# Kernel tuning notes

Hardware: AMD Instinct MI355X
Metric: run time of the kernel (lower is better)

## Reference

```python
import jax, jax.numpy as jnp
import numpy as np

B, S = 128, 32
C = [4, 8, 16, 32]
DN = ('NDHWC', 'DHWIO', 'NDHWC')


def _conv(x, w, stride=1, pad=None):
    k = w.shape[0]
    if pad is None:
        pad = [((k - 1) // 2, k // 2)] * 3  # k=3 -> (1,1); k=4 -> (1,2) as in scn even-kernel convention
    return jax.lax.conv_general_dilated(x, w, (stride,) * 3, pad, dimension_numbers=DN)


def _bn_relu(x, g, b, mask, eps=1e-4):
    # BatchNormLeakyReLU with leakiness=0 (ReLU); stats over ACTIVE voxels only, per channel
    cnt = jnp.maximum(mask.sum(), 1.0)
    mean = (x * mask).sum(axis=(0, 1, 2, 3)) / cnt
    var = (((x - mean) ** 2) * mask).sum(axis=(0, 1, 2, 3)) / cnt
    y = (x - mean) * jax.lax.rsqrt(var + eps) * g + b
    return jnp.maximum(y, 0.0) * mask


def _pool_mask(m):
    # scn.Convolution k=2 s=2: output site active iff any input in its 2^3 receptive field is active
    return jax.lax.reduce_window(m, 0.0, jax.lax.max, (1, 2, 2, 2, 1), (1, 2, 2, 2, 1), 'VALID')


def _up_mask(m):
    # scn.FullConvolution k=2 s=2: each active input activates its full 2^3 output block
    return jnp.repeat(jnp.repeat(jnp.repeat(m, 2, 1), 2, 2), 2, 3)


def _encoder(vox, maskraw, wp, enc, dec, wo):
    mask = (maskraw == 0).astype(vox.dtype)
    x = vox * mask
    x = _conv(x, wp) * mask  # prepare: submanifold conv 1 -> m=4
    for (g, b, ws, wd) in enc:  # 3 non-empty encoding stages (i < num_strides-1)
        x = _bn_relu(x, g, b, mask)
        x = _conv(x, ws) * mask               # submanifold conv k=3
        x = _conv(x, wd, stride=2, pad=[(0, 0)] * 3)  # strided Convolution k=2 s=2
        mask = _pool_mask(mask)
        x = x * mask
    # SparseToDense + view(-1, C*s^3) in NCDHW layout
    hidden = jnp.transpose(x, (0, 4, 1, 2, 3)).reshape(x.shape[0], -1)
    for (g, b, wu, ws3, ws4) in dec:  # i = 2, 1, 0
        x = _bn_relu(x, g, b, mask)
        x = jax.lax.conv_transpose(x, wu, (2, 2, 2), 'VALID', dimension_numbers=DN)  # FullConvolution
        mask = _up_mask(mask)
        x = x * mask
        x = _conv(x, ws3) * mask              # submanifold conv k=3 (end of decoding_conv1)
        mask = mask * (x[..., :1] > 0).astype(x.dtype)  # SparsifyFCS (applied twice; idempotent)
        x = x * mask
        x = _conv(x, ws4) * mask              # submanifold conv k=4 (decoding_conv2)
    out = _conv(x, wo) * mask                 # output: submanifold conv m -> 1
    return hidden, out


def setup_inputs():
    key = jax.random.key(0)
    ks = iter(jax.random.split(key, 64))

    def rnd(shape, s=0.1):
        return jax.random.normal(next(ks), shape, jnp.float32) * s

    inp = {}
    inp['vox'] = jax.random.normal(next(ks), (B, S, S, S, 1), jnp.float32)
    inp['maskraw'] = jax.random.randint(next(ks), (B, S, S, S, 1), 0, 10, jnp.int32)
    inp['wp'] = rnd((3, 3, 3, 1, C[0]))
    for i in range(3):
        ci, co = C[i], C[i + 1]
        inp[f'g_e{i}'] = 1.0 + rnd((ci,))
        inp[f'b_e{i}'] = rnd((ci,))
        inp[f'ws_e{i}'] = rnd((3, 3, 3, ci, ci))
        inp[f'wd_e{i}'] = rnd((2, 2, 2, ci, co))
    for j, i in enumerate([2, 1, 0]):
        ci, co = C[i + 1], C[i]
        inp[f'g_d{j}'] = 1.0 + rnd((ci,))
        inp[f'b_d{j}'] = rnd((ci,))
        inp[f'wu_d{j}'] = rnd((2, 2, 2, ci, co))
        inp[f'ws3_d{j}'] = rnd((3, 3, 3, co, co))
        inp[f'ws4_d{j}'] = rnd((4, 4, 4, co, co))
    inp['wo'] = rnd((3, 3, 3, C[0], 1))
    return inp


def reference(vox, maskraw, wp, g_e0, b_e0, ws_e0, wd_e0, g_e1, b_e1, ws_e1, wd_e1, g_e2, b_e2, ws_e2, wd_e2, g_d0, b_d0, wu_d0, ws3_d0, ws4_d0, g_d1, b_d1, wu_d1, ws3_d1, ws4_d1, g_d2, b_d2, wu_d2, ws3_d2, ws4_d2, wo):
    enc = [(g_e0, b_e0, ws_e0, wd_e0), (g_e1, b_e1, ws_e1, wd_e1), (g_e2, b_e2, ws_e2, wd_e2)]
    dec = [(g_d0, b_d0, wu_d0, ws3_d0, ws4_d0), (g_d1, b_d1, wu_d1, ws3_d1, ws4_d1), (g_d2, b_d2, wu_d2, ws3_d2, ws4_d2)]
    return _encoder(vox, maskraw, wp, enc, dec, wo)
```

## Files before the change

### kernel.cpp

```cpp
#include <hip/hip_runtime.h>

using u8 = unsigned char;

__global__ void mask_init_k(const int* __restrict__ mr, u8* __restrict__ m, int N) {
    int i = blockIdx.x * blockDim.x + threadIdx.x;
    if (i < N) m[i] = (mr[i] == 0) ? 1 : 0;
}

template <int SO>
__global__ void pool_k(const u8* __restrict__ mi, u8* __restrict__ mo) {
    const int N = 128 * SO * SO * SO;
    constexpr int SI = 2 * SO;
    int v = blockIdx.x * blockDim.x + threadIdx.x;
    if (v >= N) return;
    int t = v;
    int x = t % SO; t /= SO;
    int y = t % SO; t /= SO;
    int z = t % SO;
    int n = t / SO;
    u8 m = 0;
    for (int kd = 0; kd < 2; kd++)
        for (int kh = 0; kh < 2; kh++)
            for (int kw = 0; kw < 2; kw++)
                m |= mi[((n * SI + 2 * z + kd) * SI + 2 * y + kh) * SI + 2 * x + kw];
// ... 8 lines not shown
    int y0 = (bid & 3) << 3, z0 = ((bid >> 2) & 7) << 2, n = bid >> 5;
    for (int t = threadIdx.x; t < 6 * 10 * 35; t += 256) {
        int x_ = t % 35;
        int rr = t / 35;
        int yy = rr % 10, zz = rr / 10;
        int gx = x_ - 1, gy = y0 + yy - 1, gz = z0 + zz - 1;
        float v = 0.f;
        if ((unsigned)gx < 32u && (unsigned)gy < 32u && (unsigned)gz < 32u) {
            int gi = ((n * 32 + gz) * 32 + gy) * 32 + gx;
            if (m[gi]) v = vox[gi];
        }
        til[t] = v;
    }
    __syncthreads();
    int tx = threadIdx.x;
    int xg = tx & 7, ly = (tx >> 3) & 7, lz = tx >> 6;
    int xb = xg << 2;
    int vbase = ((n * 32 + z0 + lz) * 32 + y0 + ly) * 32 + xb;
    u8 om[4];
#pragma unroll
    for (int j = 0; j < 4; j++) om[j] = m[vbase + j];
    float acc[4][4];
#pragma unroll
    for (int j = 0; j < 4; j++)
#pragma unroll
        for (int co = 0; co < 4; co++) acc[j][co] = 0.f;
    for (int kd = 0; kd < 3; kd++) {
        for (int kh = 0; kh < 3; kh++) {
            const float* rowp = &til[((lz + kd) * 10 + ly + kh) * 35 + xb];
            float col[6];
#pragma unroll
            for (int c = 0; c < 6; c++) col[c] = rowp[c];
            const float* wrow = wp + ((kd * 3 + kh) * 3) * 4;
#pragma unroll
            for (int kw = 0; kw < 3; kw++) {
                const float* wt = wrow + kw * 4;
#pragma unroll
                for (int j = 0; j < 4; j++) {
                    float xv = col[j + kw];
#pragma unroll
                    for (int co = 0; co < 4; co++) acc[j][co] += xv * wt[co];
                }
            }
        }
    }
#pragma unroll
    for (int j = 0; j < 4; j++) {
        float4 o = make_float4(om[j] ? acc[j][0] : 0.f, om[j] ? acc[j][1] : 0.f,
                               om[j] ? acc[j][2] : 0.f, om[j] ? acc[j][3] : 0.f);
        *(float4*)(out + (size_t)(vbase + j) * 4) = o;
    }
}

__global__ void convbn4t_k(const float* __restrict__ in, const float* __restrict__ w,
                           const u8* __restrict__ mask, const double* __restrict__ params,
                           float* __restrict__ out) {
    __shared__ float4 til[6 * 10 * 35];
    float sc[4], sh[4];
#pragma unroll
    for (int c = 0; c < 4; c++) { sc[c] = (float)params[c]; sh[c] = (float)params[4 + c]; }
    int bid = blockIdx.x;
    int y0 = (bid & 3) << 3, z0 = ((bid >> 2) & 7) << 2, n = bid >> 5;
    for (int t = threadIdx.x; t < 6 * 10 * 35; t += 256) {
        int x_ = t % 35;
        int rr = t / 35;
        int yy = rr % 10, zz = rr / 10;
        int gx = x_ - 1, gy = y0 + yy - 1, gz = z0 + zz - 1;
        float4 v = make_float4(0.f, 0.f, 0.f, 0.f);
        if ((unsigned)gx < 32u && (unsigned)gy < 32u && (unsigned)gz < 32u) {
            int gi = ((n * 32 + gz) * 32 + gy) * 32 + gx;
            if (mask[gi]) {
                float4 r = *(const float4*)(in + (size_t)gi * 4);
                v.x = fmaxf(r.x * sc[0] + sh[0], 0.f);
                v.y = fmaxf(r.y * sc[1] + sh[1], 0.f);
                v.z = fmaxf(r.z * sc[2] + sh[2], 0.f);
                v.w = fmaxf(r.w * sc[3] + sh[3], 0.f);
            }
        }
        til[t] = v;
    }
    __syncthreads();
    int tx = threadIdx.x;
    int xg = tx & 7, ly = (tx >> 3) & 7, lz = tx >> 6;
    int xb = xg << 2;
    int vbase = ((n * 32 + z0 + lz) * 32 + y0 + ly) * 32 + xb;
    u8 om[4];
#pragma unroll
    for (int j = 0; j < 4; j++) om[j] = mask[vbase + j];
    float acc[4][4];
#pragma unroll
    for (int j = 0; j < 4; j++)
#pragma unroll
        for (int co = 0; co < 4; co++) acc[j][co] = 0.f;
    for (int kd = 0; kd < 3; kd++) {
        for (int kh = 0; kh < 3; kh++) {
            const float4* rowp = &til[((lz + kd) * 10 + ly + kh) * 35 + xb];
            float col[6][4];
#pragma unroll
            for (int c = 0; c < 6; c++) {
                float4 t4 = rowp[c];
                col[c][0] = t4.x; col[c][1] = t4.y; col[c][2] = t4.z; col[c][3] = t4.w;
            }
            const float* wrow = w + ((kd * 3 + kh) * 3) * 16;
#pragma unroll
            for (int kw = 0; kw < 3; kw++) {
                const float* wt = wrow + kw * 16;
#pragma unroll
                for (int j = 0; j < 4; j++) {
#pragma unroll
                    for (int ci = 0; ci < 4; ci++) {
                        float xv = col[j + kw][ci];
#pragma unroll
                        for (int co = 0; co < 4; co++) acc[j][co] += xv * wt[ci * 4 + co];
                    }
                }
            }
        }
    }
#pragma unroll
    for (int j = 0; j < 4; j++) {
        float4 o = make_float4(om[j] ? acc[j][0] : 0.f, om[j] ? acc[j][1] : 0.f,
                               om[j] ? acc[j][2] : 0.f, om[j] ? acc[j][3] : 0.f);
        *(float4*)(out + (size_t)(vbase + j) * 4) = o;
    }
}

__global__ void conv3s4t_k(const float* __restrict__ in, const float* __restrict__ w,
                           const u8* __restrict__ pmask, u8* __restrict__ nmask,
                           float* __restrict__ out) {
    __shared__ float4 til[6 * 10 * 35];
    int bid = blockIdx.x;
    int y0 = (bid & 3) << 3, z0 = ((bid >> 2) & 7) << 2, n = bid >> 5;
    for (int t = threadIdx.x; t < 6 * 10 * 35; t += 256) {
        int x_ = t % 35;
        int rr = t / 35;
        int yy = rr % 10, zz = rr / 10;
        int gx = x_ - 1, gy = y0 + yy - 1, gz = z0 + zz - 1;
        float4 v = make_float4(0.f, 0.f, 0.f, 0.f);
        if ((unsigned)gx < 32u && (unsigned)gy < 32u && (unsigned)gz < 32u)
            v = *(const float4*)(in + (size_t)(((n * 32 + gz) * 32 + gy) * 32 + gx) * 4);
        til[t] = v;
    }
    __syncthreads();
    int tx = threadIdx.x;
    int xg = tx & 7, ly = (tx >> 3) & 7, lz = tx >> 6;
    int xb = xg << 2;
    int gy = y0 + ly, gz = z0 + lz;
    int vbase = ((n * 32 + gz) * 32 + gy) * 32 + xb;
    int pbase = ((n * 16 + (gz >> 1)) * 16 + (gy >> 1)) * 16 + (xb >> 1);
    u8 pm[4];
    pm[0] = pm[1] = pmask[pbase];
    pm[2] = pm[3] = pmask[pbase + 1];
    double acc0[4];
    float accf[4][4];
#pragma unroll
    for (int j = 0; j < 4; j++) {
        acc0[j] = 0.0;
#pragma unroll
        for (int co = 0; co < 4; co++) accf[j][co] = 0.f;
    }
    for (int kd = 0; kd < 3; kd++) {
        for (int kh = 0; kh < 3; kh++) {
            const float4* rowp = &til[((lz + kd) * 10 + ly + kh) * 35 + xb];
            float col[6][4];
#pragma unroll
            for (int c = 0; c < 6; c++) {
                float4 t4 = rowp[c];
                col[c][0] = t4.x; col[c][1] = t4.y; col[c][2] = t4.z; col[c][3] = t4.w;
            }
            const float* wrow = w + ((kd * 3 + kh) * 3) * 16;
#pragma unroll
            for (int kw = 0; kw < 3; kw++) {
                const float* wt = wrow + kw * 16;
#pragma unroll
                for (int j = 0; j < 4; j++) {
#pragma unroll
                    for (int ci = 0; ci < 4; ci++) {
                        float xv = col[j + kw][ci];
                        acc0[j] += (double)xv * (double)wt[ci * 4 + 0];
#pragma unroll
                        for (int co = 1; co < 4; co++) accf[j][co] += xv * wt[ci * 4 + co];
                    }
                }
            }
        }
    }
    unsigned nm4 = 0;
#pragma unroll
    for (int j = 0; j < 4; j++) {
        u8 nm = (pm[j] && (acc0[j] > 0.0)) ? 1 : 0;
        nm4 |= ((unsigned)nm) << (8 * j);
        float4 o = make_float4(nm ? (float)acc0[j] : 0.f, nm ? accf[j][1] : 0.f,
                               nm ? accf[j][2] : 0.f, nm ? accf[j][3] : 0.f);
// ... 64 lines not shown
}

__global__ void outconv4t_k(const float* __restrict__ in, const float* __restrict__ w,
                            const u8* __restrict__ mask, float* __restrict__ out) {
    __shared__ float4 til[6 * 10 * 35];
    int bid = blockIdx.x;
    int y0 = (bid & 3) << 3, z0 = ((bid >> 2) & 7) << 2, n = bid >> 5;
    for (int t = threadIdx.x; t < 6 * 10 * 35; t += 256) {
        int x_ = t % 35;
        int rr = t / 35;
        int yy = rr % 10, zz = rr / 10;
        int gx = x_ - 1, gy = y0 + yy - 1, gz = z0 + zz - 1;
        float4 v = make_float4(0.f, 0.f, 0.f, 0.f);
        if ((unsigned)gx < 32u && (unsigned)gy < 32u && (unsigned)gz < 32u)
            v = *(const float4*)(in + (size_t)(((n * 32 + gz) * 32 + gy) * 32 + gx) * 4);
        til[t] = v;
    }
    __syncthreads();
    int tx = threadIdx.x;
    int xg = tx & 7, ly = (tx >> 3) & 7, lz = tx >> 6;
    int xb = xg << 2;
    int vbase = ((n * 32 + z0 + lz) * 32 + y0 + ly) * 32 + xb;
    u8 om[4];
#pragma unroll
    for (int j = 0; j < 4; j++) om[j] = mask[vbase + j];
    float acc[4] = {0.f, 0.f, 0.f, 0.f};
    for (int kd = 0; kd < 3; kd++) {
        for (int kh = 0; kh < 3; kh++) {
            const float4* rowp = &til[((lz + kd) * 10 + ly + kh) * 35 + xb];
            float col[6][4];
#pragma unroll
            for (int c = 0; c < 6; c++) {
                float4 t4 = rowp[c];
                col[c][0] = t4.x; col[c][1] = t4.y; col[c][2] = t4.z; col[c][3] = t4.w;
            }
            const float* wrow = w + ((kd * 3 + kh) * 3) * 4;
#pragma unroll
            for (int kw = 0; kw < 3; kw++) {
                const float* wt = wrow + kw * 4;
#pragma unroll
                for (int j = 0; j < 4; j++) {
#pragma unroll
                    for (int ci = 0; ci < 4; ci++) acc[j] += col[j + kw][ci] * wt[ci];
                }
            }
        }
    }
    float4 o = make_float4(om[0] ? acc[0] : 0.f, om[1] ? acc[1] : 0.f,
                           om[2] ? acc[2] : 0.f, om[3] ? acc[3] : 0.f);
    *(float4*)(out + vbase) = o;
}


__global__ void convbn16t_k(const float* __restrict__ in, const float* __restrict__ w,
                            const u8* __restrict__ mask, const double* __restrict__ params,
                            float* __restrict__ out) {
    __shared__ float4 til[2][1140];
    __shared__ float wl[1728];
    float sc[8], sh[8];
#pragma unroll
    for (int c = 0; c < 8; c++) { sc[c] = (float)params[c]; sh[c] = (float)params[8 + c]; }
    int bid = blockIdx.x;
    int y0 = (bid & 1) << 3, z0 = ((bid >> 1) & 3) << 2, n = bid >> 3;
    for (int t = threadIdx.x; t < 1728; t += 256) wl[t] = w[t];
    for (int t = threadIdx.x; t < 1140; t += 256) {
        int x_ = t % 19;
        int rr = t / 19;
        int yy = rr % 10, zz = rr / 10;
        int gx = x_ - 1, gy = y0 + yy - 1, gz = z0 + zz - 1;
        float v[8];
#pragma unroll
        for (int c = 0; c < 8; c++) v[c] = 0.f;
        if ((unsigned)gx < 16u && (unsigned)gy < 16u && (unsigned)gz < 16u) {
            int gi = ((n * 16 + gz) * 16 + gy) * 16 + gx;
            if (mask[gi]) {
                const float* ip = in + (size_t)gi * 8;
#pragma unroll
                for (int c = 0; c < 8; c++) v[c] = fmaxf(ip[c] * sc[c] + sh[c], 0.f);
            }
        }
        til[0][t] = make_float4(v[0], v[1], v[2], v[3]);
        til[1][t] = make_float4(v[4], v[5], v[6], v[7]);
    }
    __syncthreads();
    int xg = threadIdx.x & 7, ly = (threadIdx.x >> 3) & 7, lz = threadIdx.x >> 6;
    int xb = xg << 1;
    int vbase = ((n * 16 + z0 + lz) * 16 + y0 + ly) * 16 + xb;
    u8 om[2] = {mask[vbase], mask[vbase + 1]};
    float acc[2][8];
#pragma unroll
    for (int j = 0; j < 2; j++)
#pragma unroll
        for (int co = 0; co < 8; co++) acc[j][co] = 0.f;
    for (int kd = 0; kd < 3; kd++) {
        for (int kh = 0; kh < 3; kh++) {
            int rbase = ((lz + kd) * 10 + ly + kh) * 19 + xb;
            float col[4][8];
#pragma unroll
            for (int c = 0; c < 4; c++) {
                float4 a = til[0][rbase + c], b = til[1][rbase + c];
                col[c][0] = a.x; col[c][1] = a.y; col[c][2] = a.z; col[c][3] = a.w;
                col[c][4] = b.x; col[c][5] = b.y; col[c][6] = b.z; col[c][7] = b.w;
            }
            const float* wrow = wl + ((kd * 3 + kh) * 3) * 64;
#pragma unroll
            for (int kw = 0; kw < 3; kw++) {
                const float* wt = wrow + kw * 64;
#pragma unroll
                for (int j = 0; j < 2; j++) {
#pragma unroll
                    for (int ci = 0; ci < 8; ci++) {
                        float xv = col[j + kw][ci];
#pragma unroll
                        for (int co = 0; co < 8; co++) acc[j][co] += xv * wt[ci * 8 + co];
                    }
                }
            }
        }
    }
#pragma unroll
    for (int j = 0; j < 2; j++) {
        float* op = out + (size_t)(vbase + j) * 8;
        float4 o0 = make_float4(om[j] ? acc[j][0] : 0.f, om[j] ? acc[j][1] : 0.f,
                                om[j] ? acc[j][2] : 0.f, om[j] ? acc[j][3] : 0.f);
        float4 o1 = make_float4(om[j] ? acc[j][4] : 0.f, om[j] ? acc[j][5] : 0.f,
                                om[j] ? acc[j][6] : 0.f, om[j] ? acc[j][7] : 0.f);
        ((float4*)op)[0] = o0;
        ((float4*)op)[1] = o1;
    }
}

__global__ void conv3s16t_k(const float* __restrict__ in, const float* __restrict__ w,
                            const u8* __restrict__ pmask, u8* __restrict__ nmask,
                            float* __restrict__ out, double delta) {
    __shared__ float4 til[2][1140];
    __shared__ float wl[1728];
    int bid = blockIdx.x;
    int y0 = (bid & 1) << 3, z0 = ((bid >> 1) & 3) << 2, n = bid >> 3;
    for (int t = threadIdx.x; t < 1728; t += 256) wl[t] = w[t];
    for (int t = threadIdx.x; t < 1140; t += 256) {
        int x_ = t % 19;
        int rr = t / 19;
        int yy = rr % 10, zz = rr / 10;
        int gx = x_ - 1, gy = y0 + yy - 1, gz = z0 + zz - 1;
        float4 a = make_float4(0.f, 0.f, 0.f, 0.f), b = a;
        if ((unsigned)gx < 16u && (unsigned)gy < 16u && (unsigned)gz < 16u) {
            const float4* ip = (const float4*)(in + (size_t)(((n * 16 + gz) * 16 + gy) * 16 + gx) * 8);
            a = ip[0]; b = ip[1];
        }
        til[0][t] = a;
        til[1][t] = b;
    }
    __syncthreads();
    int xg = threadIdx.x & 7, ly = (threadIdx.x >> 3) & 7, lz = threadIdx.x >> 6;
    int xb = xg << 1;
    int gy = y0 + ly, gz = z0 + lz;
    int vbase = ((n * 16 + gz) * 16 + gy) * 16 + xb;
    u8 pm = pmask[((n * 8 + (gz >> 1)) * 8 + (gy >> 1)) * 8 + (xb >> 1)];
    double acc0[2], asum[2];
    float accf[2][8];
#pragma unroll
    for (int j = 0; j < 2; j++) {
        acc0[j] = 0.0; asum[j] = 0.0;
#pragma unroll
        for (int co = 0; co < 8; co++) accf[j][co] = 0.f;
    }
    for (int kd = 0; kd < 3; kd++) {
        for (int kh = 0; kh < 3; kh++) {
            int rbase = ((lz + kd) * 10 + ly + kh) * 19 + xb;
            float col[4][8];
#pragma unroll
            for (int c = 0; c < 4; c++) {
                float4 a = til[0][rbase + c], b = til[1][rbase + c];
                col[c][0] = a.x; col[c][1] = a.y; col[c][2] = a.z; col[c][3] = a.w;
                col[c][4] = b.x; col[c][5] = b.y; col[c][6] = b.z; col[c][7] = b.w;
            }
            const float* wrow = wl + ((kd * 3 + kh) * 3) * 64;
#pragma unroll
            for (int kw = 0; kw < 3; kw++) {
                const float* wt = wrow + kw * 64;
#pragma unroll
                for (int j = 0; j < 2; j++) {
#pragma unroll
                    for (int ci = 0; ci < 8; ci++) {
                        float xv = col[j + kw][ci];
                        double term = (double)xv * (double)wt[ci * 8 + 0];
                        acc0[j] += term;
                        asum[j] += fabs(term);
#pragma unroll
                        for (int co = 1; co < 8; co++) accf[j][co] += xv * wt[ci * 8 + co];
                    }
                }
            }
        }
    }
    unsigned short nm2 = 0;
#pragma unroll
    for (int j = 0; j < 2; j++) {
        u8 nm = (pm && (acc0[j] > -delta * asum[j])) ? 1 : 0;
        nm2 |= ((unsigned short)nm) << (8 * j);
        float* op = out + (size_t)(vbase + j) * 8;
        float4 o0 = make_float4(nm ? (float)acc0[j] : 0.f, nm ? accf[j][1] : 0.f,
                                nm ? accf[j][2] : 0.f, nm ? accf[j][3] : 0.f);
        float4 o1 = make_float4(nm ? accf[j][4] : 0.f, nm ? accf[j][5] : 0.f,
// ... 86 lines not shown
    for (int t = threadIdx.x; t < 27 * 256; t += 256) wl[t] = w[t];
    for (int t = threadIdx.x; t < 300; t += 256) {
        int xx = t % 10;
        int rr = t / 10;
        int yy = rr % 10, zz = rr / 10;
        int gx = xx - 1, gy = yy - 1, gz = z + zz - 1;
        float v[16];
#pragma unroll
        for (int c = 0; c < 16; c++) v[c] = 0.f;
        if ((unsigned)gx < 8u && (unsigned)gy < 8u && (unsigned)gz < 8u) {
            int gi = ((n * 8 + gz) * 8 + gy) * 8 + gx;
            if (mask[gi]) {
                const float* ip = in + (size_t)gi * 16;
#pragma unroll
                for (int c = 0; c < 16; c++) v[c] = fmaxf(ip[c] * sc[c] + sh[c], 0.f);
            }
        }
        int s = (zz * 10 + yy) * 11 + xx;
#pragma unroll
        for (int q = 0; q < 4; q++)
            til[q][s] = make_float4(v[4 * q], v[4 * q + 1], v[4 * q + 2], v[4 * q + 3]);
    }
    __syncthreads();
    int x = threadIdx.x & 7, y = (threadIdx.x >> 3) & 7, cq = threadIdx.x >> 6;
    int v = ((n * 8 + z) * 8 + y) * 8 + x;
    u8 om = mask[v];
    float acc[4] = {0.f, 0.f, 0.f, 0.f};
    for (int kd = 0; kd < 3; kd++) {
        for (int kh = 0; kh < 3; kh++) {
            int rbase = (kd * 10 + y + kh) * 11 + x;
            const float* wrow = wl + ((kd * 3 + kh) * 3) * 256;
#pragma unroll
            for (int kw = 0; kw < 3; kw++) {
                int s = rbase + kw;
                float4 q0 = til[0][s], q1 = til[1][s], q2 = til[2][s], q3 = til[3][s];
                float xs[16] = {q0.x, q0.y, q0.z, q0.w, q1.x, q1.y, q1.z, q1.w,
                                q2.x, q2.y, q2.z, q2.w, q3.x, q3.y, q3.z, q3.w};
                const float* wt = wrow + kw * 256 + cq * 4;
#pragma unroll
                for (int ci = 0; ci < 16; ci++) {
                    float xv = xs[ci];
                    float4 w4 = *(const float4*)(wt + ci * 16);
                    acc[0] += xv * w4.x; acc[1] += xv * w4.y;
                    acc[2] += xv * w4.z; acc[3] += xv * w4.w;
                }
            }
        }
    }
    float4 o = make_float4(om ? acc[0] : 0.f, om ? acc[1] : 0.f,
                           om ? acc[2] : 0.f, om ? acc[3] : 0.f);
    *(float4*)(out + (size_t)v * 16 + cq * 4) = o;
}

__global__ void conv3s8_k(const float* __restrict__ in, const float* __restrict__ w,
                          const u8* __restrict__ pmask, u8* __restrict__ nmask,
                          float* __restrict__ out, double delta) {
    __shared__ float4 til[4][330];
    __shared__ float wl[27 * 256];
    __shared__ u8 nmsh[64];
    int z = blockIdx.x & 7, n = blockIdx.x >> 3;
    for (int t = threadIdx.x; t < 27 * 256; t += 256) wl[t] = w[t];
    for (int t = threadIdx.x; t < 300; t += 256) {
        int xx = t % 10;
        int rr = t / 10;
        int yy = rr % 10, zz = rr / 10;
        int gx = xx - 1, gy = yy - 1, gz = z + zz - 1;
        float4 v0 = make_float4(0.f, 0.f, 0.f, 0.f), v1 = v0, v2 = v0, v3 = v0;
        if ((unsigned)gx < 8u && (unsigned)gy < 8u && (unsigned)gz < 8u) {
            const float4* ip = (const float4*)(in + (size_t)(((n * 8 + gz) * 8 + gy) * 8 + gx) * 16);
            v0 = ip[0]; v1 = ip[1]; v2 = ip[2]; v3 = ip[3];
        }
        int s = (zz * 10 + yy) * 11 + xx;
        til[0][s] = v0; til[1][s] = v1; til[2][s] = v2; til[3][s] = v3;
    }
    __syncthreads();
    int x = threadIdx.x & 7, y = (threadIdx.x >> 3) & 7, cq = threadIdx.x >> 6;
    int v = ((n * 8 + z) * 8 + y) * 8 + x;
    double acc0 = 0.0, asum = 0.0;
    float acc[4] = {0.f, 0.f, 0.f, 0.f};
    for (int kd = 0; kd < 3; kd++) {
        for (int kh = 0; kh < 3; kh++) {
            int rbase = (kd * 10 + y + kh) * 11 + x;
            const float* wrow = wl + ((kd * 3 + kh) * 3) * 256;
#pragma unroll
            for (int kw = 0; kw < 3; kw++) {
                int s = rbase + kw;
                float4 q0 = til[0][s], q1 = til[1][s], q2 = til[2][s], q3 = til[3][s];
                float xs[16] = {q0.x, q0.y, q0.z, q0.w, q1.x, q1.y, q1.z, q1.w,
                                q2.x, q2.y, q2.z, q2.w, q3.x, q3.y, q3.z, q3.w};
                const float* wt0 = wrow + kw * 256;
                if (cq == 0) {
#pragma unroll
                    for (int ci = 0; ci < 16; ci++) {
                        float xv = xs[ci];
                        double term = (double)xv * (double)wt0[ci * 16];
                        acc0 += term;
                        asum += fabs(term);
#pragma unroll
                        for (int j = 1; j < 4; j++) acc[j] += xv * wt0[ci * 16 + j];
                    }
                } else {
                    const float* wt = wt0 + cq * 4;
#pragma unroll
                    for (int ci = 0; ci < 16; ci++) {
                        float xv = xs[ci];
                        float4 w4 = *(const float4*)(wt + ci * 16);
                        acc[0] += xv * w4.x; acc[1] += xv * w4.y;
                        acc[2] += xv * w4.z; acc[3] += xv * w4.w;
                    }
                }
            }
        }
    }
    if (cq == 0) {
        u8 pm = pmask[((n * 4 + (z >> 1)) * 4 + (y >> 1)) * 4 + (x >> 1)];
        u8 nm = (pm && (acc0 > -delta * asum)) ? 1 : 0;
        nmsh[y * 8 + x] = nm;
        nmask[v] = nm;
    }
    __syncthreads();
    u8 nm = nmsh[y * 8 + x];
    float4 o;
    if (cq == 0) {
        o = make_float4(nm ? (float)acc0 : 0.f, nm ? acc[1] : 0.f,
                        nm ? acc[2] : 0.f, nm ? acc[3] : 0.f);
    } else {
// ... 38 lines not shown
                float4 q0 = til[0][s], q1 = til[1][s], q2 = til[2][s], q3 = til[3][s];
                float xs[16] = {q0.x, q0.y, q0.z, q0.w, q1.x, q1.y, q1.z, q1.w,
                                q2.x, q2.y, q2.z, q2.w, q3.x, q3.y, q3.z, q3.w};
                const float* wt = wrow + kw * 256 + cq * 4;
#pragma unroll
                for (int ci = 0; ci < 16; ci++) {
                    float xv = xs[ci];
                    float4 w4 = *(const float4*)(wt + ci * 16);
                    acc[0] += xv * w4.x; acc[1] += xv * w4.y;
                    acc[2] += xv * w4.z; acc[3] += xv * w4.w;
                }
            }
        }
    }
    float4 o = make_float4(om ? acc[0] : 0.f, om ? acc[1] : 0.f,
                           om ? acc[2] : 0.f, om ? acc[3] : 0.f);
    *(float4*)(out + (size_t)v * 16 + cq * 4) = o;
}


template <int CIN, int COUT, int SO>
__global__ void down_k(const float* __restrict__ in, const float* __restrict__ w,
                       const u8* __restrict__ outmask, float* __restrict__ out) {
    const int N = 128 * SO * SO * SO;
    constexpr int SI = 2 * SO;
    int v = blockIdx.x * blockDim.x + threadIdx.x;
    if (v >= N) return;
    if (!outmask[v]) {
#pragma unroll
        for (int co = 0; co < COUT; co++) out[(size_t)v * COUT + co] = 0.f;
        return;
    }
    int t = v;
    int x = t % SO; t /= SO;
    int y = t % SO; t /= SO;
    int z = t % SO;
    int n = t / SO;
    float acc[COUT];
#pragma unroll
    for (int co = 0; co < COUT; co++) acc[co] = 0.f;
    for (int kd = 0; kd < 2; kd++)
        for (int kh = 0; kh < 2; kh++)
            for (int kw = 0; kw < 2; kw++) {
                int sv = ((n * SI + 2 * z + kd) * SI + 2 * y + kh) * SI + 2 * x + kw;
                const float* ip = in + (size_t)sv * CIN;
                const float* wpk = w + ((kd * 2 + kh) * 2 + kw) * CIN * COUT;
#pragma unroll
                for (int ci = 0; ci < CIN; ci++) {
                    float xv = ip[ci];
#pragma unroll
                    for (int co = 0; co < COUT; co++) acc[co] += xv * wpk[ci * COUT + co];
                }
            }
#pragma unroll
    for (int co = 0; co < COUT; co++) out[(size_t)v * COUT + co] = acc[co];
}

template <int CIN, int COUT, int SI>
__global__ void upbn_k(const float* __restrict__ in, const float* __restrict__ w,
                       const u8* __restrict__ inmask, const double* __restrict__ params,
                       float* __restrict__ out) {
    constexpr int SO = 2 * SI;
    const int N = 128 * SO * SO * SO;
    int v = blockIdx.x * blockDim.x + threadIdx.x;
    if (v >= N) return;
    int t = v;
    int x = t % SO; t /= SO;
    int y = t % SO; t /= SO;
    int z = t % SO;
    int n = t / SO;
    int sv = ((n * SI + (z >> 1)) * SI + (y >> 1)) * SI + (x >> 1);
    if (!inmask[sv]) {
#pragma unroll
        for (int co = 0; co < COUT; co++) out[(size_t)v * COUT + co] = 0.f;
        return;
    }
    int tap = ((1 - (z & 1)) * 2 + (1 - (y & 1))) * 2 + (1 - (x & 1));
    const float* wpk = w + tap * CIN * COUT;
    const float* ip = in + (size_t)sv * CIN;
    float acc[COUT];
#pragma unroll
    for (int co = 0; co < COUT; co++) acc[co] = 0.f;
#pragma unroll
    for (int ci = 0; ci < CIN; ci++) {
        float yv = fmaxf(ip[ci] * (float)params[ci] + (float)params[CIN + ci], 0.f);
#pragma unroll
        for (int co = 0; co < COUT; co++) acc[co] += yv * wpk[ci * COUT + co];
    }
#pragma unroll
    for (int co = 0; co < COUT; co++) out[(size_t)v * COUT + co] = acc[co];
}

template <int C>
__global__ void bn_reduce_k(const float* __restrict__ x, const u8* __restrict__ m, int N,
                            double* __restrict__ partial) {
    double cnt = 0.0, sx[C], s2[C];
#pragma unroll
    for (int c = 0; c < C; c++) { sx[c] = 0.0; s2[c] = 0.0; }
    int stride = gridDim.x * blockDim.x;
    for (int v = blockIdx.x * blockDim.x + threadIdx.x; v < N; v += stride) {
        float mk = (float)m[v];
        cnt += (double)mk;
        const float4* xp = (const float4*)(x + (size_t)v * C);
#pragma unroll
        for (int q = 0; q < C / 4; q++) {
            float4 r = xp[q];
            float f0 = r.x * mk, f1 = r.y * mk, f2 = r.z * mk, f3 = r.w * mk;
            double x0 = (double)f0, x1 = (double)f1, x2 = (double)f2, x3 = (double)f3;
            sx[4 * q + 0] += x0; s2[4 * q + 0] += x0 * x0;
            sx[4 * q + 1] += x1; s2[4 * q + 1] += x1 * x1;
            sx[4 * q + 2] += x2; s2[4 * q + 2] += x2 * x2;
            sx[4 * q + 3] += x3; s2[4 * q + 3] += x3 * x3;
        }
    }
#pragma unroll
    for (int off = 32; off > 0; off >>= 1) {
        cnt += __shfl_down(cnt, off, 64);
#pragma unroll
        for (int c = 0; c < C; c++) {
            sx[c] += __shfl_down(sx[c], off, 64);
            s2[c] += __shfl_down(s2[c], off, 64);
        }
    }
    __shared__ double sbuf[4][2 * C + 1];
    int wave = threadIdx.x >> 6;
    if ((threadIdx.x & 63) == 0) {
        sbuf[wave][0] = cnt;
#pragma unroll
        for (int c = 0; c < C; c++) {
            sbuf[wave][1 + c] = sx[c];
            sbuf[wave][1 + C + c] = s2[c];
        }
    }
    __syncthreads();
    if (threadIdx.x == 0) {
        double* p = partial + (size_t)blockIdx.x * (2 * C + 1);
        double tcnt = 0.0;
        for (int wv = 0; wv < 4; wv++) tcnt += sbuf[wv][0];
        p[0] = tcnt;
#pragma unroll
        for (int c = 0; c < C; c++) {
// ... 67 lines not shown
    const float* wu_d1 = (const float*)d_in[22];
    const float* ws3_d1 = (const float*)d_in[23];
    const float* ws4_d1 = (const float*)d_in[24];
    const float* g_d2 = (const float*)d_in[25];
    const float* b_d2 = (const float*)d_in[26];
    const float* wu_d2 = (const float*)d_in[27];
    const float* ws3_d2 = (const float*)d_in[28];
    const float* ws4_d2 = (const float*)d_in[29];
    const float* wo = (const float*)d_in[30];
    float* out = (float*)d_out;

    float* wsf = (float*)d_ws;
    size_t offf = 0;
    auto allocf = [&](size_t n) { float* p = wsf + offf; offf += n; return p; };
    float* R1 = allocf(16777216);
    float* R2 = allocf(16777216);
    float* S1 = allocf(1048576);
    float* S2 = allocf(1048576);
    float* T = allocf(262144);
    double* wsd = (double*)(wsf + offf);
    double* partial = wsd;
    double* params = wsd + 16640;
    u8* wsm = (u8*)(wsd + 16640 + 128);
    size_t offm = 0;
    auto allocm = [&](size_t n) { u8* p = wsm + offm; offm += n; return p; };
    u8* m32 = allocm(4194304);
    u8* m16 = allocm(524288);
    u8* m8 = allocm(65536);
    u8* m4 = allocm(8192);
    u8* mD8 = allocm(65536);
    u8* mD16 = allocm(524288);
    u8* mD32 = allocm(4194304);

    const int N32 = 128 * 32768;
    const int N16 = 128 * 4096;
    const int N8 = 128 * 512;
    const int N4 = 128 * 64;
    auto gs = [](int n) { return dim3((n + 255) / 256); };
    auto rbn = [](int n) { int bl = (n + 255) / 256; return bl > 256 ? 256 : bl; };
    dim3 blk(256);
    dim3 tgrid(4096);
    dim3 grid16(1024);
    dim3 grid8(1024);

    mask_init_k<<<gs(N32), blk, 0, stream>>>(mraw, m32, N32);
    pool_k<16><<<gs(N16), blk, 0, stream>>>(m32, m16);
    pool_k<8><<<gs(N8), blk, 0, stream>>>(m16, m8);
    pool_k<4><<<gs(N4), blk, 0, stream>>>(m8, m4);

    prep4t_k<<<tgrid, blk, 0, stream>>>(vox, m32, wp, R1);
    int nb0 = rbn(N32);
    bn_reduce_k<4><<<dim3(nb0), blk, 0, stream>>>(R1, m32, N32, partial);
    bn_final_k<4><<<1, 64, 0, stream>>>(partial, nb0, g_e0, b_e0, params);
    convbn4t_k<<<tgrid, blk, 0, stream>>>(R1, ws_e0, m32, params, R2);
    down_k<4, 8, 16><<<gs(N16), blk, 0, stream>>>(R2, wd_e0, m16, R1);

    int nb1 = rbn(N16);
    bn_reduce_k<8><<<dim3(nb1), blk, 0, stream>>>(R1, m16, N16, partial);
    bn_final_k<8><<<1, 64, 0, stream>>>(partial, nb1, g_e1, b_e1, params);
    convbn16t_k<<<grid16, blk, 0, stream>>>(R1, ws_e1, m16, params, R2);
    down_k<8, 16, 8><<<gs(N8), blk, 0, stream>>>(R2, wd_e1, m8, S1);

    int nb2 = rbn(N8);
    bn_reduce_k<16><<<dim3(nb2), blk, 0, stream>>>(S1, m8, N8, partial);
    bn_final_k<16><<<1, 64, 0, stream>>>(partial, nb2, g_e2, b_e2, params);
    convbn8_k<<<grid8, blk, 0, stream>>>(S1, ws_e2, m8, params, S2);
    down_k<16, 32, 4><<<gs(N4), blk, 0, stream>>>(S2, wd_e2, m4, T);

    hidden_k<<<gs(128 * 2048), blk, 0, stream>>>(T, out);

    int nb3 = rbn(N4);
    bn_reduce_k<32><<<dim3(nb3), blk, 0, stream>>>(T, m4, N4, partial);
    bn_final_k<32><<<1, 64, 0, stream>>>(partial, nb3, g_d0, b_d0, params);
    upbn_k<32, 16, 4><<<gs(N8), blk, 0, stream>>>(T, wu_d0, m4, params, S1);
    conv3s8_k<<<grid8, blk, 0, stream>>>(S1, ws3_d0, m4, mD8, S2, 4e-7);
    conv48_k<<<grid8, blk, 0, stream>>>(S2, ws4_d0, mD8, S1);

    int nb4 = rbn(N8);
    bn_reduce_k<16><<<dim3(nb4), blk, 0, stream>>>(S1, mD8, N8, partial);
    bn_final_k<16><<<1, 64, 0, stream>>>(partial, nb4, g_d1, b_d1, params);
    upbn_k<16, 8, 8><<<gs(N16), blk, 0, stream>>>(S1, wu_d1, mD8, params, R1);
    conv3s16t_k<<<grid16, blk, 0, stream>>>(R1, ws3_d1, mD8, mD16, R2, 4e-7);
    conv416t_k<<<grid16, blk, 0, stream>>>(R2, ws4_d1, mD16, R1);

    int nb5 = rbn(N16);
    bn_reduce_k<8><<<dim3(nb5), blk, 0, stream>>>(R1, mD16, N16, partial);
    bn_final_k<8><<<1, 64, 0, stream>>>(partial, nb5, g_d2, b_d2, params);
    upbn_k<8, 4, 16><<<gs(N32), blk, 0, stream>>>(R1, wu_d2, mD16, params, R2);
    conv3s4t_k<<<tgrid, blk, 0, stream>>>(R2, ws3_d2, mD16, mD32, R1);
    conv4x4t_k<<<tgrid, blk, 0, stream>>>(R1, ws4_d2, mD32, R2);
    outconv4t_k<<<tgrid, blk, 0, stream>>>(R2, wo, mD32, out + 262144);
}
```

Measured before the change: 1.297 ms.

## Fuse strided downsample into conv epilogue and upsample into conv tile load

The encoder submanifold conv kernels now keep their output tile in shared memory and apply the 2x2x2 stride-2 downsampling conv in place, so the full-resolution intermediate is never written. The decoder's transposed-conv with BN+ReLU is recomputed inside the following conv's halo tile load, which removes the separate upbn kernels and their full-resolution round trip. The price is redundant upsample arithmetic on halo voxels and extra shared-memory syncs. Only half of the threads do the downsample work, and buffer assignments are reshuffled to match.

```diff
diff --git a/kernel.cpp b/kernel.cpp
--- a/kernel.cpp
+++ b/kernel.cpp
@@ -84,9 +84,10 @@
     }
 }
 
-__global__ void convbn4t_k(const float* __restrict__ in, const float* __restrict__ w,
-                           const u8* __restrict__ mask, const double* __restrict__ params,
-                           float* __restrict__ out) {
+__global__ void convbndown4t_k(const float* __restrict__ in, const float* __restrict__ w,
+                               const u8* __restrict__ mask, const double* __restrict__ params,
+                               const float* __restrict__ wd, const u8* __restrict__ m16,
+                               float* __restrict__ out16) {
     __shared__ float4 til[6 * 10 * 35];
     float sc[4], sh[4];
 #pragma unroll
@@ -149,18 +150,51 @@
             }
         }
     }
+    __syncthreads();
+    int ridx = (lz * 8 + ly) * 32 + xb;
 #pragma unroll
     for (int j = 0; j < 4; j++) {
-        float4 o = make_float4(om[j] ? acc[j][0] : 0.f, om[j] ? acc[j][1] : 0.f,
-                               om[j] ? acc[j][2] : 0.f, om[j] ? acc[j][3] : 0.f);
-        *(float4*)(out + (size_t)(vbase + j) * 4) = o;
-    }
-}
-
-__global__ void conv3s4t_k(const float* __restrict__ in, const float* __restrict__ w,
-                           const u8* __restrict__ pmask, u8* __restrict__ nmask,
-                           float* __restrict__ out) {
+        til[ridx + j] = make_float4(om[j] ? acc[j][0] : 0.f, om[j] ? acc[j][1] : 0.f,
+                                    om[j] ? acc[j][2] : 0.f, om[j] ? acc[j][3] : 0.f);
+    }
+    __syncthreads();
+    if (tx < 128) {
+        int ox = tx & 15, oy = (tx >> 4) & 3, oz = tx >> 6;
+        int y16 = (y0 >> 1) + oy, z16 = (z0 >> 1) + oz;
+        int v16 = ((n * 16 + z16) * 16 + y16) * 16 + ox;
+        float acc8[8];
+#pragma unroll
+        for (int co = 0; co < 8; co++) acc8[co] = 0.f;
+        if (m16[v16]) {
+            for (int kd = 0; kd < 2; kd++)
+                for (int kh = 0; kh < 2; kh++)
+#pragma unroll
+                    for (int kw = 0; kw < 2; kw++) {
+                        float4 f = til[(((2 * oz + kd) * 8 + 2 * oy + kh) * 32) + 2 * ox + kw];
+                        const float* wpk = wd + ((kd * 2 + kh) * 2 + kw) * 32;
+                        float xs[4] = {f.x, f.y, f.z, f.w};
+#pragma unroll
+                        for (int ci = 0; ci < 4; ci++) {
+                            float xv = xs[ci];
+#pragma unroll
+                            for (int co = 0; co < 8; co++) acc8[co] += xv * wpk[ci * 8 + co];
+                        }
+                    }
+        }
+        float* op = out16 + (size_t)v16 * 8;
+        ((float4*)op)[0] = make_float4(acc8[0], acc8[1], acc8[2], acc8[3]);
+        ((float4*)op)[1] = make_float4(acc8[4], acc8[5], acc8[6], acc8[7]);
+    }
+}
+
+__global__ void conv3s4tf_k(const float* __restrict__ in16, const float* __restrict__ wu,
+                            const float* __restrict__ w, const u8* __restrict__ pmask,
+                            u8* __restrict__ nmask, float* __restrict__ out,
+                            const double* __restrict__ params) {
     __shared__ float4 til[6 * 10 * 35];
+    float sc[8], sh[8];
+#pragma unroll
+    for (int c = 0; c < 8; c++) { sc[c] = (float)params[c]; sh[c] = (float)params[8 + c]; }
     int bid = blockIdx.x;
     int y0 = (bid & 3) << 3, z0 = ((bid >> 2) & 7) << 2, n = bid >> 5;
     for (int t = threadIdx.x; t < 6 * 10 * 35; t += 256) {
@@ -169,8 +203,22 @@
         int yy = rr % 10, zz = rr / 10;
         int gx = x_ - 1, gy = y0 + yy - 1, gz = z0 + zz - 1;
         float4 v = make_float4(0.f, 0.f, 0.f, 0.f);
-        if ((unsigned)gx < 32u && (unsigned)gy < 32u && (unsigned)gz < 32u)
-            v = *(const float4*)(in + (size_t)(((n * 32 + gz) * 32 + gy) * 32 + gx) * 4);
+        if ((unsigned)gx < 32u && (unsigned)gy < 32u && (unsigned)gz < 32u) {
+            int p16 = ((n * 16 + (gz >> 1)) * 16 + (gy >> 1)) * 16 + (gx >> 1);
+            if (pmask[p16]) {
+                int tap = ((1 - (gz & 1)) * 2 + (1 - (gy & 1))) * 2 + (1 - (gx & 1));
+                const float* ip = in16 + (size_t)p16 * 8;
+                const float* wt = wu + tap * 32;
+#pragma unroll
+                for (int ci = 0; ci < 8; ci++) {
+                    float yv = fmaxf(ip[ci] * sc[ci] + sh[ci], 0.f);
+                    v.x += yv * wt[ci * 4 + 0];
+                    v.y += yv * wt[ci * 4 + 1];
+                    v.z += yv * wt[ci * 4 + 2];
+                    v.w += yv * wt[ci * 4 + 3];
+                }
+            }
+        }
         til[t] = v;
     }
     __syncthreads();
@@ -341,9 +389,10 @@
 }
 
 
-__global__ void convbn16t_k(const float* __restrict__ in, const float* __restrict__ w,
-                            const u8* __restrict__ mask, const double* __restrict__ params,
-                            float* __restrict__ out) {
+__global__ void convbndown16t_k(const float* __restrict__ in, const float* __restrict__ w,
+                                const u8* __restrict__ mask, const double* __restrict__ params,
+                                const float* __restrict__ wd, const u8* __restrict__ m8,
+                                float* __restrict__ out8) {
     __shared__ float4 til[2][1140];
     __shared__ float wl[1728];
     float sc[8], sh[8];
@@ -407,23 +456,58 @@
             }
         }
     }
+    __syncthreads();
+    int ridx = (lz * 8 + ly) * 16 + xb;
 #pragma unroll
     for (int j = 0; j < 2; j++) {
-        float* op = out + (size_t)(vbase + j) * 8;
-        float4 o0 = make_float4(om[j] ? acc[j][0] : 0.f, om[j] ? acc[j][1] : 0.f,
-                                om[j] ? acc[j][2] : 0.f, om[j] ? acc[j][3] : 0.f);
-        float4 o1 = make_float4(om[j] ? acc[j][4] : 0.f, om[j] ? acc[j][5] : 0.f,
-                                om[j] ? acc[j][6] : 0.f, om[j] ? acc[j][7] : 0.f);
-        ((float4*)op)[0] = o0;
-        ((float4*)op)[1] = o1;
-    }
-}
-
-__global__ void conv3s16t_k(const float* __restrict__ in, const float* __restrict__ w,
-                            const u8* __restrict__ pmask, u8* __restrict__ nmask,
-                            float* __restrict__ out, double delta) {
+        float g0 = om[j] ? acc[j][0] : 0.f, g1 = om[j] ? acc[j][1] : 0.f;
+        float g2 = om[j] ? acc[j][2] : 0.f, g3 = om[j] ? acc[j][3] : 0.f;
+        float g4 = om[j] ? acc[j][4] : 0.f, g5 = om[j] ? acc[j][5] : 0.f;
+        float g6 = om[j] ? acc[j][6] : 0.f, g7 = om[j] ? acc[j][7] : 0.f;
+        til[0][ridx + j] = make_float4(g0, g1, g2, g3);
+        til[1][ridx + j] = make_float4(g4, g5, g6, g7);
+    }
+    __syncthreads();
+    int tx = threadIdx.x;
+    if (tx < 128) {
+        int ox = tx & 7, oy = (tx >> 3) & 3, oz = (tx >> 5) & 1, cq2 = tx >> 6;
+        int y8 = (y0 >> 1) + oy, z8 = (z0 >> 1) + oz;
+        int v8 = ((n * 8 + z8) * 8 + y8) * 8 + ox;
+        float acc16[8];
+#pragma unroll
+        for (int co = 0; co < 8; co++) acc16[co] = 0.f;
+        if (m8[v8]) {
+            for (int kd = 0; kd < 2; kd++)
+                for (int kh = 0; kh < 2; kh++)
+#pragma unroll
+                    for (int kw = 0; kw < 2; kw++) {
+                        int si = (((2 * oz + kd) * 8 + 2 * oy + kh) * 16) + 2 * ox + kw;
+                        float4 a = til[0][si], b = til[1][si];
+                        float xs[8] = {a.x, a.y, a.z, a.w, b.x, b.y, b.z, b.w};
+                        const float* wpk = wd + ((kd * 2 + kh) * 2 + kw) * 128 + cq2 * 8;
+#pragma unroll
+                        for (int ci = 0; ci < 8; ci++) {
+                            float xv = xs[ci];
+#pragma unroll
+                            for (int co = 0; co < 8; co++) acc16[co] += xv * wpk[ci * 16 + co];
+                        }
+                    }
+        }
+        float* op = out8 + (size_t)v8 * 16 + cq2 * 8;
+        ((float4*)op)[0] = make_float4(acc16[0], acc16[1], acc16[2], acc16[3]);
+        ((float4*)op)[1] = make_float4(acc16[4], acc16[5], acc16[6], acc16[7]);
+    }
+}
+
+__global__ void conv3s16tf_k(const float* __restrict__ in8, const float* __restrict__ wu,
+                             const float* __restrict__ w, const u8* __restrict__ pmask,
+                             u8* __restrict__ nmask, float* __restrict__ out,
+                             const double* __restrict__ params, double delta) {
     __shared__ float4 til[2][1140];
     __shared__ float wl[1728];
+    float sc[16], sh[16];
+#pragma unroll
+    for (int c = 0; c < 16; c++) { sc[c] = (float)params[c]; sh[c] = (float)params[16 + c]; }
     int bid = blockIdx.x;
     int y0 = (bid & 1) << 3, z0 = ((bid >> 1) & 3) << 2, n = bid >> 3;
     for (int t = threadIdx.x; t < 1728; t += 256) wl[t] = w[t];
@@ -432,13 +516,25 @@
         int rr = t / 19;
         int yy = rr % 10, zz = rr / 10;
         int gx = x_ - 1, gy = y0 + yy - 1, gz = z0 + zz - 1;
-        float4 a = make_float4(0.f, 0.f, 0.f, 0.f), b = a;
+        float v[8];
+#pragma unroll
+        for (int c = 0; c < 8; c++) v[c] = 0.f;
         if ((unsigned)gx < 16u && (unsigned)gy < 16u && (unsigned)gz < 16u) {
-            const float4* ip = (const float4*)(in + (size_t)(((n * 16 + gz) * 16 + gy) * 16 + gx) * 8);
-            a = ip[0]; b = ip[1];
-        }
-        til[0][t] = a;
-        til[1][t] = b;
+            int p8 = ((n * 8 + (gz >> 1)) * 8 + (gy >> 1)) * 8 + (gx >> 1);
+            if (pmask[p8]) {
+                int tap = ((1 - (gz & 1)) * 2 + (1 - (gy & 1))) * 2 + (1 - (gx & 1));
+                const float* ip = in8 + (size_t)p8 * 16;
+                const float* wt = wu + tap * 128;
+#pragma unroll
+                for (int ci = 0; ci < 16; ci++) {
+                    float yv = fmaxf(ip[ci] * sc[ci] + sh[ci], 0.f);
+#pragma unroll
+                    for (int co = 0; co < 8; co++) v[co] += yv * wt[ci * 8 + co];
+                }
+            }
+        }
+        til[0][t] = make_float4(v[0], v[1], v[2], v[3]);
+        til[1][t] = make_float4(v[4], v[5], v[6], v[7]);
     }
     __syncthreads();
     int xg = threadIdx.x & 7, ly = (threadIdx.x >> 3) & 7, lz = threadIdx.x >> 6;
@@ -631,12 +727,16 @@
     *(float4*)(out + (size_t)v * 16 + cq * 4) = o;
 }
 
-__global__ void conv3s8_k(const float* __restrict__ in, const float* __restrict__ w,
-                          const u8* __restrict__ pmask, u8* __restrict__ nmask,
-                          float* __restrict__ out, double delta) {
+__global__ void conv3s8f_k(const float* __restrict__ in4, const float* __restrict__ wu,
+                           const float* __restrict__ w, const u8* __restrict__ pmask,
+                           u8* __restrict__ nmask, float* __restrict__ out,
+                           const double* __restrict__ params, double delta) {
     __shared__ float4 til[4][330];
     __shared__ float wl[27 * 256];
     __shared__ u8 nmsh[64];
+    float sc[32], sh[32];
+#pragma unroll
+    for (int c = 0; c < 32; c++) { sc[c] = (float)params[c]; sh[c] = (float)params[32 + c]; }
     int z = blockIdx.x & 7, n = blockIdx.x >> 3;
     for (int t = threadIdx.x; t < 27 * 256; t += 256) wl[t] = w[t];
     for (int t = threadIdx.x; t < 300; t += 256) {
@@ -644,13 +744,27 @@
         int rr = t / 10;
         int yy = rr % 10, zz = rr / 10;
         int gx = xx - 1, gy = yy - 1, gz = z + zz - 1;
-        float4 v0 = make_float4(0.f, 0.f, 0.f, 0.f), v1 = v0, v2 = v0, v3 = v0;
+        float v[16];
+#pragma unroll
+        for (int c = 0; c < 16; c++) v[c] = 0.f;
         if ((unsigned)gx < 8u && (unsigned)gy < 8u && (unsigned)gz < 8u) {
-            const float4* ip = (const float4*)(in + (size_t)(((n * 8 + gz) * 8 + gy) * 8 + gx) * 16);
-            v0 = ip[0]; v1 = ip[1]; v2 = ip[2]; v3 = ip[3];
+            int p4 = ((n * 4 + (gz >> 1)) * 4 + (gy >> 1)) * 4 + (gx >> 1);
+            if (pmask[p4]) {
+                int tap = ((1 - (gz & 1)) * 2 + (1 - (gy & 1))) * 2 + (1 - (gx & 1));
+                const float* ip = in4 + (size_t)p4 * 32;
+                const float* wt = wu + tap * 512;
+#pragma unroll
+                for (int ci = 0; ci < 32; ci++) {
+                    float yv = fmaxf(ip[ci] * sc[ci] + sh[ci], 0.f);
+#pragma unroll
+                    for (int co = 0; co < 16; co++) v[co] += yv * wt[ci * 16 + co];
+                }
+            }
         }
         int s = (zz * 10 + yy) * 11 + xx;
-        til[0][s] = v0; til[1][s] = v1; til[2][s] = v2; til[3][s] = v3;
+#pragma unroll
+        for (int q = 0; q < 4; q++)
+            til[q][s] = make_float4(v[4 * q], v[4 * q + 1], v[4 * q + 2], v[4 * q + 3]);
     }
     __syncthreads();
     int x = threadIdx.x & 7, y = (threadIdx.x >> 3) & 7, cq = threadIdx.x >> 6;
@@ -795,41 +909,6 @@
                     for (int co = 0; co < COUT; co++) acc[co] += xv * wpk[ci * COUT + co];
                 }
             }
-#pragma unroll
-    for (int co = 0; co < COUT; co++) out[(size_t)v * COUT + co] = acc[co];
-}
-
-template <int CIN, int COUT, int SI>
-__global__ void upbn_k(const float* __restrict__ in, const float* __restrict__ w,
-                       const u8* __restrict__ inmask, const double* __restrict__ params,
-                       float* __restrict__ out) {
-    constexpr int SO = 2 * SI;
-    const int N = 128 * SO * SO * SO;
-    int v = blockIdx.x * blockDim.x + threadIdx.x;
-    if (v >= N) return;
-    int t = v;
-    int x = t % SO; t /= SO;
-    int y = t % SO; t /= SO;
-    int z = t % SO;
-    int n = t / SO;
-    int sv = ((n * SI + (z >> 1)) * SI + (y >> 1)) * SI + (x >> 1);
-    if (!inmask[sv]) {
-#pragma unroll
-        for (int co = 0; co < COUT; co++) out[(size_t)v * COUT + co] = 0.f;
-        return;
-    }
-    int tap = ((1 - (z & 1)) * 2 + (1 - (y & 1))) * 2 + (1 - (x & 1));
-    const float* wpk = w + tap * CIN * COUT;
-    const float* ip = in + (size_t)sv * CIN;
-    float acc[COUT];
-#pragma unroll
-    for (int co = 0; co < COUT; co++) acc[co] = 0.f;
-#pragma unroll
-    for (int ci = 0; ci < CIN; ci++) {
-        float yv = fmaxf(ip[ci] * (float)params[ci] + (float)params[CIN + ci], 0.f);
-#pragma unroll
-        for (int co = 0; co < COUT; co++) acc[co] += yv * wpk[ci * COUT + co];
-    }
 #pragma unroll
     for (int co = 0; co < COUT; co++) out[(size_t)v * COUT + co] = acc[co];
 }
@@ -1003,14 +1082,12 @@
     int nb0 = rbn(N32);
     bn_reduce_k<4><<<dim3(nb0), blk, 0, stream>>>(R1, m32, N32, partial);
     bn_final_k<4><<<1, 64, 0, stream>>>(partial, nb0, g_e0, b_e0, params);
-    convbn4t_k<<<tgrid, blk, 0, stream>>>(R1, ws_e0, m32, params, R2);
-    down_k<4, 8, 16><<<gs(N16), blk, 0, stream>>>(R2, wd_e0, m16, R1);
+    convbndown4t_k<<<tgrid, blk, 0, stream>>>(R1, ws_e0, m32, params, wd_e0, m16, R2);
 
     int nb1 = rbn(N16);
-    bn_reduce_k<8><<<dim3(nb1), blk, 0, stream>>>(R1, m16, N16, partial);
+    bn_reduce_k<8><<<dim3(nb1), blk, 0, stream>>>(R2, m16, N16, partial);
     bn_final_k<8><<<1, 64, 0, stream>>>(partial, nb1, g_e1, b_e1, params);
-    convbn16t_k<<<grid16, blk, 0, stream>>>(R1, ws_e1, m16, params, R2);
-    down_k<8, 16, 8><<<gs(N8), blk, 0, stream>>>(R2, wd_e1, m8, S1);
+    convbndown16t_k<<<grid16, blk, 0, stream>>>(R2, ws_e1, m16, params, wd_e1, m8, S1);
 
     int nb2 = rbn(N8);
     bn_reduce_k<16><<<dim3(nb2), blk, 0, stream>>>(S1, m8, N8, partial);
@@ -1023,22 +1100,19 @@
     int nb3 = rbn(N4);
     bn_reduce_k<32><<<dim3(nb3), blk, 0, stream>>>(T, m4, N4, partial);
     bn_final_k<32><<<1, 64, 0, stream>>>(partial, nb3, g_d0, b_d0, params);
-    upbn_k<32, 16, 4><<<gs(N8), blk, 0, stream>>>(T, wu_d0, m4, params, S1);
-    conv3s8_k<<<grid8, blk, 0, stream>>>(S1, ws3_d0, m4, mD8, S2, 4e-7);
+    conv3s8f_k<<<grid8, blk, 0, stream>>>(T, wu_d0, ws3_d0, m4, mD8, S2, params, 4e-7);
     conv48_k<<<grid8, blk, 0, stream>>>(S2, ws4_d0, mD8, S1);
 
     int nb4 = rbn(N8);
     bn_reduce_k<16><<<dim3(nb4), blk, 0, stream>>>(S1, mD8, N8, partial);
     bn_final_k<16><<<1, 64, 0, stream>>>(partial, nb4, g_d1, b_d1, params);
-    upbn_k<16, 8, 8><<<gs(N16), blk, 0, stream>>>(S1, wu_d1, mD8, params, R1);
-    conv3s16t_k<<<grid16, blk, 0, stream>>>(R1, ws3_d1, mD8, mD16, R2, 4e-7);
+    conv3s16tf_k<<<grid16, blk, 0, stream>>>(S1, wu_d1, ws3_d1, mD8, mD16, R2, params, 4e-7);
     conv416t_k<<<grid16, blk, 0, stream>>>(R2, ws4_d1, mD16, R1);
 
     int nb5 = rbn(N16);
     bn_reduce_k<8><<<dim3(nb5), blk, 0, stream>>>(R1, mD16, N16, partial);
     bn_final_k<8><<<1, 64, 0, stream>>>(partial, nb5, g_d2, b_d2, params);
-    upbn_k<8, 4, 16><<<gs(N32), blk, 0, stream>>>(R1, wu_d2, mD16, params, R2);
-    conv3s4t_k<<<tgrid, blk, 0, stream>>>(R2, ws3_d2, mD16, mD32, R1);
-    conv4x4t_k<<<tgrid, blk, 0, stream>>>(R1, ws4_d2, mD32, R2);
-    outconv4t_k<<<tgrid, blk, 0, stream>>>(R2, wo, mD32, out + 262144);
-}
+    conv3s4tf_k<<<tgrid, blk, 0, stream>>>(R1, wu_d2, ws3_d2, mD16, mD32, R2, params);
+    conv4x4t_k<<<tgrid, blk, 0, stream>>>(R2, ws4_d2, mD32, R1);
+    outconv4t_k<<<tgrid, blk, 0, stream>>>(R1, wo, mD32, out + 262144);
+}
```

After: 1.389 ms. +7.1%, slower.
